# Kernel optimization log

Measured on AMD Instinct MI355X. Metric: run time of the kernel, lower is better.

## Reference

```python
import jax, jax.numpy as jnp
import numpy as np

N, E, D, H, G = 50000, 1_600_000, 13, 32, 128
EPS = 1e-5


def _lin(k, fan_in, fan_out):
    kw, kb = jax.random.split(k)
    bound = 1.0 / np.sqrt(fan_in)
    W = jax.random.uniform(kw, (fan_in, fan_out), jnp.float32, -bound, bound)
    b = jax.random.uniform(kb, (fan_out,), jnp.float32, -bound, bound)
    return W, b


def setup_inputs() -> dict:
    key = jax.random.key(0)
    ks = jax.random.split(key, 10)
    x = jax.random.normal(ks[0], (N, D), jnp.float32)
    edge_index = jax.random.randint(ks[1], (2, E), 0, N)
    batch = jnp.sort(jax.random.randint(ks[2], (N,), 0, G))
    bn_gamma = jnp.ones((D,), jnp.float32)
    bn_beta = jnp.zeros((D,), jnp.float32)
    in_w1, in_b1 = _lin(ks[3], D, H)
    in_w2, in_b2 = _lin(ks[4], H, H)
    conv_w1, conv_b1 = _lin(ks[5], 2 * (H + D), 2 * H)
    conv_w2, conv_b2 = _lin(ks[6], 2 * H, H)
    out_w1, out_b1 = _lin(ks[7], H + D, H)
    out_w2, out_b2 = _lin(ks[8], H, 1)
    return dict(x=x, edge_index=edge_index, batch=batch,
                bn_gamma=bn_gamma, bn_beta=bn_beta,
                in_w1=in_w1, in_b1=in_b1, in_w2=in_w2, in_b2=in_b2,
                conv_w1=conv_w1, conv_b1=conv_b1, conv_w2=conv_w2, conv_b2=conv_b2,
                out_w1=out_w1, out_b1=out_b1, out_w2=out_w2, out_b2=out_b2)


def reference(x, edge_index, batch, bn_gamma, bn_beta,
              in_w1, in_b1, in_w2, in_b2,
              conv_w1, conv_b1, conv_w2, conv_b2,
              out_w1, out_b1, out_w2, out_b2):
    # BatchNorm1d (training-mode batch statistics, biased variance)
    mu = jnp.mean(x, axis=0)
    var = jnp.mean((x - mu) ** 2, axis=0)
    X = (x - mu) / jnp.sqrt(var + EPS) * bn_gamma + bn_beta  # [N, D]
    # inputnet
    Hn = jnp.tanh(jax.nn.relu(X @ in_w1 + in_b1) @ in_w2 + in_b2)  # [N, H]
    feat = jnp.concatenate([Hn, X], axis=-1)  # [N, H+D]
    # n_iters = 1 EdgeConv iteration: message = nn([x_i, x_j - x_i]), aggr='add' at target i
    src, dst = edge_index[0], edge_index[1]
    x_i = feat[dst]                               # [E, H+D] target
    x_j = feat[src]                               # [E, H+D] source
    m = jnp.concatenate([x_i, x_j - x_i], axis=-1)  # [E, 2(H+D)]
    m = jnp.tanh(jax.nn.relu(m @ conv_w1 + conv_b1) @ conv_w2 + conv_b2)  # [E, H]
    Hn = jax.ops.segment_sum(m, dst, num_segments=N)  # [N, H]
    feat = jnp.concatenate([Hn, X], axis=-1)  # [N, H+D]
    # global_mean_pool over graphs
    sums = jax.ops.segment_sum(feat, batch, num_segments=G)  # [G, H+D]
    counts = jax.ops.segment_sum(jnp.ones((feat.shape[0], 1), feat.dtype), batch, num_segments=G)
    x_mean = sums / jnp.maximum(counts, 1.0)
    # outputnet
    return jax.nn.sigmoid(jax.nn.relu(x_mean @ out_w1 + out_b1) @ out_w2 + out_b2)  # [G, 1]
```

## Files before the change

kernel.cpp:

```cpp
#include <hip/hip_runtime.h>


typedef __attribute__((ext_vector_type(4))) float floatx4;
typedef __attribute__((ext_vector_type(8))) short short8;

__device__ __forceinline__ unsigned short f2bf(float f) {
    unsigned int u = __float_as_uint(f);
    u += 0x7FFFu + ((u >> 16) & 1u);
    return (unsigned short)(u >> 16);
}
__device__ __forceinline__ float bf2f(unsigned short u) {
    return __uint_as_float(((unsigned int)u) << 16);
}
__device__ __forceinline__ float fast_tanh(float x) {
    float ax = fminf(fabsf(x), 20.0f);
    float t = __expf(-2.0f * ax);
    float r = (1.0f - t) / (1.0f + t);
    return copysignf(r, x);
}
__device__ __forceinline__ float fast_sigmoid(float x) {
    float xc = fminf(fmaxf(x, -30.f), 30.f);
    return 1.0f / (1.0f + __expf(-xc));
}
__device__ __forceinline__ void atomic_pk_add_bf16(unsigned short* addr, unsigned int packed) {
    asm volatile("global_atomic_pk_add_bf16 %0, %1, off" :: "v"(addr), "v"(packed) : "memory");
}

#define NBLK_STAT 120

__global__ __launch_bounds__(256) void k_bnstat(const float* __restrict__ x, int N,
                                                float* __restrict__ part,
                                                uint4* __restrict__ HnZ, int hnq,
                                                float* __restrict__ gacc, int gn) {
    int tid = blockIdx.x * blockDim.x + threadIdx.x;
    int stride = gridDim.x * blockDim.x;
    uint4 z4 = make_uint4(0u, 0u, 0u, 0u);
    for (int i = tid; i < hnq; i += stride) HnZ[i] = z4;
    for (int i = tid; i < gn; i += stride) gacc[i] = 0.f;

    float s[13], q[13];
#pragma unroll
    for (int d = 0; d < 13; d++) { s[d] = 0.f; q[d] = 0.f; }
    for (int n = tid; n < N; n += stride) {
        const float* row = x + (size_t)n * 13;
#pragma unroll
        for (int d = 0; d < 13; d++) { float f = row[d]; s[d] += f; q[d] += f * f; }
    }
#pragma unroll
    for (int d = 0; d < 13; d++) {
        for (int off = 32; off > 0; off >>= 1) {
            s[d] += __shfl_down(s[d], off, 64);
            q[d] += __shfl_down(q[d], off, 64);
        }
    }
    __shared__ float red[4][26];
    int w = threadIdx.x >> 6;
    if ((threadIdx.x & 63) == 0) {
#pragma unroll
        for (int d = 0; d < 13; d++) { red[w][d] = s[d]; red[w][13 + d] = q[d]; }
    }
    __syncthreads();
    if (threadIdx.x < 26) {
        float v = red[0][threadIdx.x] + red[1][threadIdx.x] + red[2][threadIdx.x] + red[3][threadIdx.x];
        int d = threadIdx.x;
        if (d < 13) part[blockIdx.x * 32 + d] = v;
        else        part[NBLK_STAT * 32 + blockIdx.x * 32 + (d - 13)] = v;
    }
}

#define FP 72
#define WP 72
__global__ __launch_bounds__(128) void k_node(
    const float* __restrict__ x, const int* __restrict__ batch,
    const float* __restrict__ bn_g, const float* __restrict__ bn_b,
    const float* __restrict__ in_w1, const float* __restrict__ in_b1,
    const float* __restrict__ in_w2, const float* __restrict__ in_b2,
    const float* __restrict__ conv_w1, const float* __restrict__ conv_b1,
    const float* __restrict__ part,
    unsigned short* __restrict__ A, unsigned short* __restrict__ Bm,
    float* __restrict__ gacc, int N) {
    __shared__ float sW1[13 * 32], sB1[32], sW2[32 * 32], sB2[32];
    __shared__ float sScl[16], sShf[16];
    __shared__ unsigned short sWcatT[128 * WP];
    __shared__ unsigned short sFeat[128 * FP];
    int tid = threadIdx.x;

    for (int i = tid; i < 13 * 32; i += 128) sW1[i] = in_w1[i];
    if (tid < 32) { sB1[tid] = in_b1[tid]; sB2[tid] = in_b2[tid]; }
    for (int i = tid; i < 32 * 32; i += 128) sW2[i] = in_w2[i];
    for (int i = tid; i < 128 * 64; i += 128) {
        int c = i >> 6, k = i & 63;
        float v = 0.f;
        if (k < 45) {
            int cc = c & 63;
            float bot = conv_w1[(45 + k) * 64 + cc];
            v = (c < 64) ? (conv_w1[k * 64 + cc] - bot) : bot;
        }
        sWcatT[c * WP + k] = f2bf(v);
    }
    if (tid < 13) {
        float su = 0.f, sq = 0.f;
        for (int b = 0; b < NBLK_STAT; b++) {
            su += part[b * 32 + tid];
            sq += part[NBLK_STAT * 32 + b * 32 + tid];
        }
        float invN = 1.0f / (float)N;
        float mu = su * invN;
        float var = fmaxf(sq * invN - mu * mu, 0.f);
        float sc = bn_g[tid] / sqrtf(var + 1e-5f);
        sScl[tid] = sc;
        sShf[tid] = bn_b[tid] - mu * sc;
    }
    __syncthreads();

    int n = blockIdx.x * 128 + tid;
    bool valid = (n < N);
    int nl = valid ? n : (N - 1);

    float X[13];
#pragma unroll
    for (int d = 0; d < 13; d++)
        X[d] = x[(size_t)nl * 13 + d] * sScl[d] + sShf[d];
    float h1[32];
#pragma unroll
    for (int j = 0; j < 32; j++) {
        float acc = sB1[j];
#pragma unroll
        for (int d = 0; d < 13; d++) acc += X[d] * sW1[d * 32 + j];
        h1[j] = fmaxf(acc, 0.f);
    }
    float h2[32];
#pragma unroll
    for (int j = 0; j < 32; j++) {
        float acc = sB2[j];
#pragma unroll
        for (int k = 0; k < 32; k++) acc += h1[k] * sW2[k * 32 + j];
        h2[j] = fast_tanh(acc);
    }

    unsigned int fw[16];
#pragma unroll
    for (int i = 0; i < 16; i++) fw[i] = 0;
    if (valid) {
#pragma unroll
        for (int i = 0; i < 16; i++)
            fw[i] = (unsigned)f2bf(h2[2 * i]) | ((unsigned)f2bf(h2[2 * i + 1]) << 16);
    }
    unsigned int xw[7];
#pragma unroll
    for (int i = 0; i < 7; i++) xw[i] = 0;
    if (valid) {
#pragma unroll
        for (int i = 0; i < 6; i++)
            xw[i] = (unsigned)f2bf(X[2 * i]) | ((unsigned)f2bf(X[2 * i + 1]) << 16);
        xw[6] = (unsigned)f2bf(X[12]);
    }
    {
        unsigned short* row = sFeat + tid * FP;
        ((uint4*)row)[0] = make_uint4(fw[0], fw[1], fw[2], fw[3]);
        ((uint4*)row)[1] = make_uint4(fw[4], fw[5], fw[6], fw[7]);
        ((uint4*)row)[2] = make_uint4(fw[8], fw[9], fw[10], fw[11]);
        ((uint4*)row)[3] = make_uint4(fw[12], fw[13], fw[14], fw[15]);
        ((uint4*)row)[4] = make_uint4(xw[0], xw[1], xw[2], xw[3]);
        ((uint4*)row)[5] = make_uint4(xw[4], xw[5], xw[6], 0u);
        ((uint4*)row)[6] = make_uint4(0u, 0u, 0u, 0u);
        ((uint4*)row)[7] = make_uint4(0u, 0u, 0u, 0u);
    }

    {
        int g = valid ? batch[n] : -1;
        unsigned long long uni = __ballot(g == __shfl(g, 0, 64));
        if (uni == ~0ull && g >= 0) {
            float red[14];
#pragma unroll
            for (int d = 0; d < 13; d++) red[d] = X[d];
            red[13] = 1.0f;
#pragma unroll
            for (int d = 0; d < 14; d++)
                for (int off = 32; off > 0; off >>= 1)
                    red[d] += __shfl_down(red[d], off, 64);
            if ((tid & 63) == 0) {
#pragma unroll
                for (int d = 0; d < 13; d++) unsafeAtomicAdd(&gacc[g * 46 + 32 + d], red[d]);
                unsafeAtomicAdd(&gacc[g * 46 + 45], red[13]);
            }
        } else if (valid) {
#pragma unroll
            for (int d = 0; d < 13; d++) unsafeAtomicAdd(&gacc[g * 46 + 32 + d], X[d]);
            unsafeAtomicAdd(&gacc[g * 46 + 45], 1.0f);
        }
    }
    __syncthreads();

    int lane = tid & 63;
    int w = tid >> 6;
    int q = lane >> 4;
    int m = lane & 15;

    short8 wf[2][8];
#pragma unroll
    for (int ks = 0; ks < 2; ks++)
#pragma unroll
        for (int t = 0; t < 8; t++) {
            wf[ks][t] = *(const short8*)(sWcatT + (t * 16 + m) * WP + ks * 32 + q * 8);
        }
    float cb1v[4];
#pragma unroll
    for (int t = 0; t < 4; t++) cb1v[t] = conv_b1[t * 16 + m];

    int base = blockIdx.x * 128 + w * 64;
#pragma unroll
    for (int tile = 0; tile < 4; tile++) {
        const unsigned short* ar = sFeat + (w * 64 + tile * 16 + m) * FP;
        short8 a0 = *(const short8*)(ar + q * 8);
        short8 a1 = *(const short8*)(ar + 32 + q * 8);
        floatx4 c[8];
#pragma unroll
        for (int t = 0; t < 8; t++) {
            floatx4 z = {0.f, 0.f, 0.f, 0.f};
            c[t] = __builtin_amdgcn_mfma_f32_16x16x32_bf16(a0, wf[0][t], z, 0, 0, 0);
            c[t] = __builtin_amdgcn_mfma_f32_16x16x32_bf16(a1, wf[1][t], c[t], 0, 0, 0);
        }
#pragma unroll
        for (int r = 0; r < 4; r++) {
            int row = base + tile * 16 + (q << 2) + r;
            if (row < N) {
#pragma unroll
                for (int t = 0; t < 4; t++)
                    A[(size_t)row * 64 + t * 16 + m] = f2bf(c[t][r] + cb1v[t]);
#pragma unroll
                for (int t = 4; t < 8; t++)
                    Bm[(size_t)row * 64 + (t - 4) * 16 + m] = f2bf(c[t][r]);
            }
        }
    }
}

__global__ __launch_bounds__(256) void k_edge(
    const int* __restrict__ ei,
    const unsigned short* __restrict__ A, const unsigned short* __restrict__ Bm,
    const float* __restrict__ conv_w2, const float* __restrict__ conv_b2,
    unsigned short* __restrict__ Hn, int E) {
    int lane = threadIdx.x & 63;
    int wid  = blockIdx.x * (blockDim.x >> 6) + (threadIdx.x >> 6);
    int nw   = gridDim.x * (blockDim.x >> 6);
    int q = lane >> 4;
    int m = lane & 15;

    short8 wf[2][2];
#pragma unroll
    for (int s = 0; s < 2; s++)
#pragma unroll
        for (int t = 0; t < 2; t++)
#pragma unroll
            for (int j = 0; j < 8; j++)
                wf[s][t][j] = (short)f2bf(conv_w2[(s * 32 + q * 8 + j) * 32 + 2 * m + t]);
    float cb2a = conv_b2[2 * m];
    float cb2b = conv_b2[2 * m + 1];

    const int* srcp = ei;
    const int* dstp = ei + E;
    int npairs = E >> 5;

    for (int p = wid; p < npairs; p += nw) {
        int e0 = p << 5;
        int vd0 = dstp[e0 + m];
        int vs0 = srcp[e0 + m];
        int vd1 = dstp[e0 + 16 + m];
        int vs1 = srcp[e0 + 16 + m];
        uint4 av0a = *(const uint4*)(A  + (size_t)vd0 * 64 + q * 8);
        uint4 av0b = *(const uint4*)(A  + (size_t)vd0 * 64 + 32 + q * 8);
        uint4 bv0a = *(const uint4*)(Bm + (size_t)vs0 * 64 + q * 8);
        uint4 bv0b = *(const uint4*)(Bm + (size_t)vs0 * 64 + 32 + q * 8);
        uint4 av1a = *(const uint4*)(A  + (size_t)vd1 * 64 + q * 8);
        uint4 av1b = *(const uint4*)(A  + (size_t)vd1 * 64 + 32 + q * 8);
        uint4 bv1a = *(const uint4*)(Bm + (size_t)vs1 * 64 + q * 8);
        uint4 bv1b = *(const uint4*)(Bm + (size_t)vs1 * 64 + 32 + q * 8);

        floatx4 c00 = {0.f, 0.f, 0.f, 0.f}, c01 = {0.f, 0.f, 0.f, 0.f};
        floatx4 c10 = {0.f, 0.f, 0.f, 0.f}, c11 = {0.f, 0.f, 0.f, 0.f};

        auto mk = [](uint4 av, uint4 bv) -> short8 {
            unsigned au[4] = {av.x, av.y, av.z, av.w};
            unsigned bu[4] = {bv.x, bv.y, bv.z, bv.w};
            short8 ha;
#pragma unroll
            for (int i = 0; i < 4; i++) {
                float a0 = __uint_as_float(au[i] << 16);
                float a1 = __uint_as_float(au[i] & 0xffff0000u);
                float b0 = __uint_as_float(bu[i] << 16);
                float b1 = __uint_as_float(bu[i] & 0xffff0000u);
                float h0 = fmaxf(a0 + b0, 0.f);
                float h1v = fmaxf(a1 + b1, 0.f);
                ha[2 * i]     = (short)(f2bf(h0));
                ha[2 * i + 1] = (short)(f2bf(h1v));
            }
            return ha;
        };
        short8 h0a = mk(av0a, bv0a);
        short8 h0b = mk(av0b, bv0b);
        short8 h1a = mk(av1a, bv1a);
        short8 h1b = mk(av1b, bv1b);

        c00 = __builtin_amdgcn_mfma_f32_16x16x32_bf16(h0a, wf[0][0], c00, 0, 0, 0);
        c01 = __builtin_amdgcn_mfma_f32_16x16x32_bf16(h0a, wf[0][1], c01, 0, 0, 0);
        c10 = __builtin_amdgcn_mfma_f32_16x16x32_bf16(h1a, wf[0][0], c10, 0, 0, 0);
        c11 = __builtin_amdgcn_mfma_f32_16x16x32_bf16(h1a, wf[0][1], c11, 0, 0, 0);
        c00 = __builtin_amdgcn_mfma_f32_16x16x32_bf16(h0b, wf[1][0], c00, 0, 0, 0);
        c01 = __builtin_amdgcn_mfma_f32_16x16x32_bf16(h0b, wf[1][1], c01, 0, 0, 0);
        c10 = __builtin_amdgcn_mfma_f32_16x16x32_bf16(h1b, wf[1][0], c10, 0, 0, 0);
        c11 = __builtin_amdgcn_mfma_f32_16x16x32_bf16(h1b, wf[1][1], c11, 0, 0, 0);

#pragma unroll
        for (int r = 0; r < 4; r++) {
            int m2 = (q << 2) + r;
            int dd0 = __shfl(vd0, m2, 64);
            int dd1 = __shfl(vd1, m2, 64);
            float o00 = fast_tanh(c00[r] + cb2a);
            float o01 = fast_tanh(c01[r] + cb2b);
            float o10 = fast_tanh(c10[r] + cb2a);
            float o11 = fast_tanh(c11[r] + cb2b);
            unsigned pk0 = (unsigned)f2bf(o00) | ((unsigned)f2bf(o01) << 16);
            unsigned pk1 = (unsigned)f2bf(o10) | ((unsigned)f2bf(o11) << 16);
            atomic_pk_add_bf16(Hn + (size_t)dd0 * 32 + 2 * m, pk0);
            atomic_pk_add_bf16(Hn + (size_t)dd1 * 32 + 2 * m, pk1);
        }
    }

    int tstart = npairs << 5;
    int tail = E - tstart;
    if (tail && wid == 0 && lane < tail) {
        int e = tstart + lane;
        int vd = dstp[e], vs = srcp[e];
        float h[64];
        for (int k = 0; k < 64; k++) {
            float a = bf2f(A[(size_t)vd * 64 + k]);
            float b = bf2f(Bm[(size_t)vs * 64 + k]);
            h[k] = fmaxf(a + b, 0.f);
        }
        for (int j = 0; j < 16; j++) {
            float acc0 = conv_b2[2 * j], acc1 = conv_b2[2 * j + 1];
            for (int k = 0; k < 64; k++) {
                acc0 += h[k] * conv_w2[k * 32 + 2 * j];
                acc1 += h[k] * conv_w2[k * 32 + 2 * j + 1];
            }
            unsigned pk = (unsigned)f2bf(fast_tanh(acc0)) | ((unsigned)f2bf(fast_tanh(acc1)) << 16);
            atomic_pk_add_bf16(Hn + (size_t)vd * 32 + 2 * j, pk);
        }
    }
}

__global__ __launch_bounds__(256) void k_pool(const unsigned short* __restrict__ Hn,
                                              const int* __restrict__ batch,
                                              float* __restrict__ gacc, int N) {
    const int NPB = 512;
    int c = threadIdx.x & 31;
    int r = threadIdx.x >> 5;
    int n0 = blockIdx.x * NPB;
    int nend = min(n0 + NPB, N);
    int gcur = -1;
    float acc = 0.f;
    for (int n = n0 + r; n < nend; n += 8) {
        int g = batch[n];
        if (g != gcur) {
            if (gcur >= 0) unsafeAtomicAdd(&gacc[gcur * 46 + c], acc);
            gcur = g; acc = 0.f;
        }
        acc += bf2f(Hn[(size_t)n * 32 + c]);
    }
    if (gcur >= 0) unsafeAtomicAdd(&gacc[gcur * 46 + c], acc);
}

__global__ void k_out(const float* __restrict__ gacc,
                      const float* __restrict__ out_w1, const float* __restrict__ out_b1,
                      const float* __restrict__ out_w2, const float* __restrict__ out_b2,
                      float* __restrict__ out, int G) {
    int g = blockIdx.x * blockDim.x + threadIdx.x;
    if (g >= G) return;
    float cnt = fmaxf(gacc[g * 46 + 45], 1.0f);
    float inv = 1.0f / cnt;
    float f[45];
#pragma unroll
    for (int i = 0; i < 45; i++) f[i] = gacc[g * 46 + i] * inv;
    float h[32];
#pragma unroll
    for (int j = 0; j < 32; j++) {
        float acc = out_b1[j];
#pragma unroll
        for (int k = 0; k < 45; k++) acc += f[k] * out_w1[k * 32 + j];
        h[j] = fmaxf(acc, 0.f);
    }
    float o = out_b2[0];
#pragma unroll
    for (int j = 0; j < 32; j++) o += h[j] * out_w2[j];
    out[g] = fast_sigmoid(o);
}

extern "C" void kernel_launch(void* const* d_in, const int* in_sizes, int n_in,
                              void* d_out, int out_size, void* d_ws, size_t ws_size,
                              hipStream_t stream) {
    const float* x      = (const float*)d_in[0];
    const int*   ei     = (const int*)d_in[1];
    const int*   batch  = (const int*)d_in[2];
    const float* bn_g   = (const float*)d_in[3];
    const float* bn_b   = (const float*)d_in[4];
    const float* in_w1  = (const float*)d_in[5];
    const float* in_b1  = (const float*)d_in[6];
    const float* in_w2  = (const float*)d_in[7];
    const float* in_b2  = (const float*)d_in[8];
    const float* cw1    = (const float*)d_in[9];
    const float* cb1    = (const float*)d_in[10];
    const float* cw2    = (const float*)d_in[11];
    const float* cb2    = (const float*)d_in[12];
    const float* ow1    = (const float*)d_in[13];
    const float* ob1    = (const float*)d_in[14];
    const float* ow2    = (const float*)d_in[15];
    const float* ob2    = (const float*)d_in[16];

    int N = in_sizes[0] / 13;
    int E = in_sizes[1] / 2;
    int G = out_size;
    int Npad = (N + 255) & ~255;

    auto al = [](size_t v) { return (v + 255) & ~(size_t)255; };
    char* ws = (char*)d_ws;
    size_t hn_off   = 0;
    size_t gacc_off = al((size_t)N * 32 * 2);
    size_t part_off = gacc_off + al((size_t)G * 46 * 4);
    size_t a_off    = part_off + al(2 * NBLK_STAT * 32 * 4);
    size_t b_off    = a_off + al((size_t)Npad * 64 * 2);

    unsigned short* Hn = (unsigned short*)(ws + hn_off);
    float* gacc = (float*)(ws + gacc_off);
    float* part = (float*)(ws + part_off);
    unsigned short* A  = (unsigned short*)(ws + a_off);
    unsigned short* Bm = (unsigned short*)(ws + b_off);

    int hnq = (N * 32 * 2) / 16;
    int gn  = G * 46;

    k_bnstat<<<NBLK_STAT, 256, 0, stream>>>(x, N, part, (uint4*)Hn, hnq, gacc, gn);
    k_node<<<(N + 127) / 128, 128, 0, stream>>>(x, batch, bn_g, bn_b,
                                                in_w1, in_b1, in_w2, in_b2,
                                                cw1, cb1, part, A, Bm, gacc, N);
    k_edge<<<2048, 256, 0, stream>>>(ei, A, Bm, cw2, cb2, Hn, E);
    k_pool<<<(N + 511) / 512, 256, 0, stream>>>(Hn, batch, gacc, N);
    k_out<<<1, 128, 0, stream>>>(gacc, ow1, ob1, ow2, ob2, (float*)d_out, G);
}
```

Baseline: 291.5 us.

## Fuse pooling and output MLP into edge kernel via last-block tickets

Removes the separate k_pool and k_out launches. The last 16 blocks to finish the edge kernel, chosen by an atomic ticket counter, each pool a slice of nodes into gacc. The last of those then runs the output MLP from shared memory. This saves two kernel launches and their gaps, but pooling now runs on only 16 blocks instead of about 98, and the final MLP runs on a single block.

```diff
diff --git a/kernel.cpp b/kernel.cpp
--- a/kernel.cpp
+++ b/kernel.cpp
@@ -240,9 +240,17 @@
     const int* __restrict__ ei,
     const unsigned short* __restrict__ A, const unsigned short* __restrict__ Bm,
     const float* __restrict__ conv_w2, const float* __restrict__ conv_b2,
-    unsigned short* __restrict__ Hn, int E) {
-    int lane = threadIdx.x & 63;
-    int wid  = blockIdx.x * (blockDim.x >> 6) + (threadIdx.x >> 6);
+    unsigned short* __restrict__ Hn, float* __restrict__ gacc,
+    int* __restrict__ counters, const int* __restrict__ batch,
+    const float* __restrict__ out_w1, const float* __restrict__ out_b1,
+    const float* __restrict__ out_w2, const float* __restrict__ out_b2,
+    float* __restrict__ out, int E, int N, int G, int nblocks) {
+    __shared__ int sTicket, sT2;
+    __shared__ float sG[128 * 46];
+
+    int tid  = threadIdx.x;
+    int lane = tid & 63;
+    int wid  = blockIdx.x * (blockDim.x >> 6) + (tid >> 6);
     int nw   = gridDim.x * (blockDim.x >> 6);
     int q = lane >> 4;
     int m = lane & 15;
@@ -348,52 +356,54 @@
             atomic_pk_add_bf16(Hn + (size_t)vd * 32 + 2 * j, pk);
         }
     }
-}
-
-__global__ __launch_bounds__(256) void k_pool(const unsigned short* __restrict__ Hn,
-                                              const int* __restrict__ batch,
-                                              float* __restrict__ gacc, int N) {
-    const int NPB = 512;
-    int c = threadIdx.x & 31;
-    int r = threadIdx.x >> 5;
-    int n0 = blockIdx.x * NPB;
-    int nend = min(n0 + NPB, N);
-    int gcur = -1;
-    float acc = 0.f;
-    for (int n = n0 + r; n < nend; n += 8) {
-        int g = batch[n];
-        if (g != gcur) {
-            if (gcur >= 0) unsafeAtomicAdd(&gacc[gcur * 46 + c], acc);
-            gcur = g; acc = 0.f;
-        }
-        acc += bf2f(Hn[(size_t)n * 32 + c]);
-    }
-    if (gcur >= 0) unsafeAtomicAdd(&gacc[gcur * 46 + c], acc);
-}
-
-__global__ void k_out(const float* __restrict__ gacc,
-                      const float* __restrict__ out_w1, const float* __restrict__ out_b1,
-                      const float* __restrict__ out_w2, const float* __restrict__ out_b2,
-                      float* __restrict__ out, int G) {
-    int g = blockIdx.x * blockDim.x + threadIdx.x;
-    if (g >= G) return;
-    float cnt = fmaxf(gacc[g * 46 + 45], 1.0f);
-    float inv = 1.0f / cnt;
-    float f[45];
-#pragma unroll
-    for (int i = 0; i < 45; i++) f[i] = gacc[g * 46 + i] * inv;
-    float h[32];
-#pragma unroll
-    for (int j = 0; j < 32; j++) {
-        float acc = out_b1[j];
-#pragma unroll
-        for (int k = 0; k < 45; k++) acc += f[k] * out_w1[k * 32 + j];
-        h[j] = fmaxf(acc, 0.f);
-    }
-    float o = out_b2[0];
-#pragma unroll
-    for (int j = 0; j < 32; j++) o += h[j] * out_w2[j];
-    out[g] = fast_sigmoid(o);
+
+    __threadfence();
+    __syncthreads();
+    if (tid == 0) sTicket = atomicAdd(&counters[0], 1);
+    __syncthreads();
+    if (sTicket < nblocks - 16) return;
+
+    {
+        int s = sTicket - (nblocks - 16);
+        int NS = (N + 15) >> 4;
+        int n0 = s * NS;
+        int n1 = min(n0 + NS, N);
+        int c = tid & 31;
+        int r = tid >> 5;
+        int gcur = -1;
+        float acc = 0.f;
+        for (int n = n0 + r; n < n1; n += 8) {
+            int g = batch[n];
+            if (g != gcur) {
+                if (gcur >= 0) unsafeAtomicAdd(&gacc[gcur * 46 + c], acc);
+                gcur = g; acc = 0.f;
+            }
+            acc += bf2f(Hn[(size_t)n * 32 + c]);
+        }
+        if (gcur >= 0) unsafeAtomicAdd(&gacc[gcur * 46 + c], acc);
+    }
+
+    __threadfence();
+    __syncthreads();
+    if (tid == 0) sT2 = atomicAdd(&counters[1], 1);
+    __syncthreads();
+    if (sT2 != 15) return;
+
+    for (int i = tid; i < G * 46; i += 256) sG[i] = gacc[i];
+    __syncthreads();
+    if (tid < G) {
+        int g = tid;
+        float cnt = fmaxf(sG[g * 46 + 45], 1.0f);
+        float inv = 1.0f / cnt;
+        float o = out_b2[0];
+        for (int j = 0; j < 32; j++) {
+            float acc = out_b1[j];
+            for (int k = 0; k < 45; k++)
+                acc += (sG[g * 46 + k] * inv) * out_w1[k * 32 + j];
+            o += fmaxf(acc, 0.f) * out_w2[j];
+        }
+        out[g] = fast_sigmoid(o);
+    }
 }
 
 extern "C" void kernel_launch(void* const* d_in, const int* in_sizes, int n_in,
@@ -426,24 +436,27 @@
     char* ws = (char*)d_ws;
     size_t hn_off   = 0;
     size_t gacc_off = al((size_t)N * 32 * 2);
-    size_t part_off = gacc_off + al((size_t)G * 46 * 4);
+    size_t part_off = gacc_off + al(((size_t)G * 46 + 16) * 4);
     size_t a_off    = part_off + al(2 * NBLK_STAT * 32 * 4);
     size_t b_off    = a_off + al((size_t)Npad * 64 * 2);
 
     unsigned short* Hn = (unsigned short*)(ws + hn_off);
     float* gacc = (float*)(ws + gacc_off);
+    int*   counters = (int*)(gacc + (size_t)G * 46);
     float* part = (float*)(ws + part_off);
     unsigned short* A  = (unsigned short*)(ws + a_off);
     unsigned short* Bm = (unsigned short*)(ws + b_off);
 
     int hnq = (N * 32 * 2) / 16;
-    int gn  = G * 46;
+    int gn  = G * 46 + 16;
+
+    const int EDGE_BLOCKS = 2048;
 
     k_bnstat<<<NBLK_STAT, 256, 0, stream>>>(x, N, part, (uint4*)Hn, hnq, gacc, gn);
     k_node<<<(N + 127) / 128, 128, 0, stream>>>(x, batch, bn_g, bn_b,
                                                 in_w1, in_b1, in_w2, in_b2,
                                                 cw1, cb1, part, A, Bm, gacc, N);
-    k_edge<<<2048, 256, 0, stream>>>(ei, A, Bm, cw2, cb2, Hn, E);
-    k_pool<<<(N + 511) / 512, 256, 0, stream>>>(Hn, batch, gacc, N);
-    k_out<<<1, 128, 0, stream>>>(gacc, ow1, ob1, ow2, ob2, (float*)d_out, G);
-}
+    k_edge<<<EDGE_BLOCKS, 256, 0, stream>>>(ei, A, Bm, cw2, cb2, Hn, gacc,
+                                            counters, batch, ow1, ob1, ow2, ob2,
+                                            (float*)d_out, E, N, G, EDGE_BLOCKS);
+}
```

After: 621.9 us. 113% more time.
